# Optimization experiments

Hardware: AMD Instinct MI355X
Metric: run time of the kernel (lower is better)

Reference implementation:

```python
import jax, jax.numpy as jnp
import numpy as np


def setup_inputs() -> dict:
    key = jax.random.key(0)
    B, N = 128, 512
    SSMap = jax.random.normal(key, (B, N, N), dtype=jnp.float32)
    return {"SSMap": SSMap}


def reference(SSMap):
    # SSMap: [B, N, N]. For each superdiagonal offset d = 1..N-2 (length L = N-d,
    # the final length-1 diagonal is excluded), compute unbiased std of
    # (diag * L / 5) = std(diag) * L / 5, then mean over diagonals per batch item.
    B, N, _ = SSMap.shape
    K = N - 2  # number of diagonals used (offsets 1..N-2)
    P = N - 1  # max diagonal length
    k = jnp.arange(K)[:, None]            # diagonal index -> offset d = k+1
    p = jnp.arange(P)[None, :]            # position along diagonal
    rows = jnp.broadcast_to(p, (K, P))    # row index i = p
    cols = p + k + 1                      # col index j = p + d
    mask = cols < N                       # valid positions: p < N - d
    cols = jnp.minimum(cols, N - 1)
    diags = SSMap[:, rows, cols]          # [B, K, P] padded diagonals
    maskf = mask.astype(SSMap.dtype)      # [K, P]
    lens = jnp.sum(maskf, axis=1)         # [K], L = N - 1 - k (>= 2)
    mean = jnp.sum(diags * maskf, axis=2) / lens            # [B, K]
    dev = (diags - mean[:, :, None]) * maskf                # masked deviations
    var = jnp.sum(dev * dev, axis=2) / (lens - 1.0)         # unbiased (ddof=1)
    scaled = jnp.sqrt(var) * lens / 5.0                     # std(diag * L / 5)
    loss = jnp.mean(scaled, axis=1)                         # [B]
    return (loss, jax.lax.stop_gradient(loss))
```

## Files before the change

kernel.cpp:

```cpp
#include <hip/hip_runtime.h>
#include <math.h>

constexpr int B_ = 128;
constexpr int N_ = 512;
constexpr int K_ = 510;

__global__ __launch_bounds__(512) void diag_partial_kernel(
    const float* __restrict__ in, float* __restrict__ ws, int split) {
  const int b = blockIdx.x / split;
  const int s = blockIdx.x % split;
  const int k = threadIdx.x;
  const float* base = in + (size_t)b * N_ * N_;
  float S = 0.0f, Q = 0.0f;
  if (k < K_) {
    const int limit = N_ - 1 - k;
    const float* ptr = base + (size_t)s * (N_ + 1) + 1 + k;
    for (int p = s; p < limit; p += split) {
      float x = *ptr;
      S += x;
      Q = fmaf(x, x, Q);
      ptr += (size_t)split * (N_ + 1);
    }
  }
  float* w = ws + (size_t)blockIdx.x * (2 * N_);
  w[k] = S;
  w[k + N_] = Q;
}

__global__ __launch_bounds__(512) void finalize_kernel(
    const float* __restrict__ ws, float* __restrict__ out, int split) {
  __shared__ float red[8];
  const int b = blockIdx.x;
  const int t = threadIdx.x;
  float Ssum = 0.0f, Qsum = 0.0f;
  for (int s = 0; s < split; ++s) {
    const float* w = ws + (size_t)(b * split + s) * (2 * N_);
    Ssum += w[t];
    Qsum += w[t + N_];
  }
  float scaled = 0.0f;
  if (t < K_) {
    float len = (float)(N_ - 1 - t);
    float mean = Ssum / len;
    float var = (Qsum - Ssum * mean) / (len - 1.0f);
    var = fmaxf(var, 0.0f);
    scaled = sqrtf(var) * len * 0.2f;
  }
  for (int off = 32; off > 0; off >>= 1)
    scaled += __shfl_down(scaled, off, 64);
  const int wid = t >> 6;
  if ((t & 63) == 0) red[wid] = scaled;
  __syncthreads();
  if (t == 0) {
    float tot = 0.0f;
    for (int i = 0; i < 8; ++i) tot += red[i];
    float loss = tot / (float)K_;
    out[b] = loss;
    out[B_ + b] = loss;
  }
}

extern "C" void kernel_launch(void* const* d_in, const int* in_sizes, int n_in,
                              void* d_out, int out_size, void* d_ws, size_t ws_size,
                              hipStream_t stream) {
  const float* in = (const float*)d_in[0];
  float* out = (float*)d_out;
  float* ws = (float*)d_ws;
  int split = 8;
  while (split > 1 &&
         (size_t)B_ * split * 2 * N_ * sizeof(float) > ws_size)
    split >>= 1;
  diag_partial_kernel<<<B_ * split, 512, 0, stream>>>(in, ws, split);
  finalize_kernel<<<B_, 512, 0, stream>>>(ws, out, split);
}
```

Baseline: 196.8 us.

## Pair long and short diagonals per thread, unroll loads, double the split

Each thread now handles two diagonals, one long (offset t+1) and one short (length t), so every thread in a block does about the same amount of work. Blocks shrink to 256 threads. The main loop is unrolled by four with separate accumulators so several independent loads are in flight at once. The split factor rises from 8 to 16 to launch more blocks, at the cost of a larger workspace and more partial sums for the finalize kernel to add up.

```diff
diff --git a/kernel.cpp b/kernel.cpp
--- a/kernel.cpp
+++ b/kernel.cpp
@@ -5,26 +5,56 @@
 constexpr int N_ = 512;
 constexpr int K_ = 510;
 
-__global__ __launch_bounds__(512) void diag_partial_kernel(
+__global__ __launch_bounds__(256) void diag_partial_kernel(
     const float* __restrict__ in, float* __restrict__ ws, int split) {
   const int b = blockIdx.x / split;
   const int s = blockIdx.x % split;
-  const int k = threadIdx.x;
+  const int t = threadIdx.x;
   const float* base = in + (size_t)b * N_ * N_;
-  float S = 0.0f, Q = 0.0f;
-  if (k < K_) {
-    const int limit = N_ - 1 - k;
-    const float* ptr = base + (size_t)s * (N_ + 1) + 1 + k;
-    for (int p = s; p < limit; p += split) {
-      float x = *ptr;
-      S += x;
-      Q = fmaf(x, x, Q);
-      ptr += (size_t)split * (N_ + 1);
+  const int la = (N_ - 1) - t;
+  const int lb = t;
+  const size_t step = (size_t)split * (N_ + 1);
+  const float* pa = base + (size_t)s * (N_ + 1) + 1 + t;
+  const float* pb = base + (size_t)s * (N_ + 1) + (N_ - t);
+  float Sa0 = 0.f, Qa0 = 0.f, Sa1 = 0.f, Qa1 = 0.f;
+  float Sb0 = 0.f, Qb0 = 0.f, Sb1 = 0.f, Qb1 = 0.f;
+  int p = s;
+  for (; p + 3 * split < la; p += 4 * split) {
+    float a0 = pa[0];
+    float a1 = pa[step];
+    float a2 = pa[2 * step];
+    float a3 = pa[3 * step];
+    float b0 = 0.f, b1 = 0.f, b2 = 0.f, b3 = 0.f;
+    if (p < lb)             b0 = pb[0];
+    if (p + split < lb)     b1 = pb[step];
+    if (p + 2 * split < lb) b2 = pb[2 * step];
+    if (p + 3 * split < lb) b3 = pb[3 * step];
+    Sa0 += a0; Qa0 = fmaf(a0, a0, Qa0);
+    Sa1 += a1; Qa1 = fmaf(a1, a1, Qa1);
+    Sa0 += a2; Qa0 = fmaf(a2, a2, Qa0);
+    Sa1 += a3; Qa1 = fmaf(a3, a3, Qa1);
+    Sb0 += b0; Qb0 = fmaf(b0, b0, Qb0);
+    Sb1 += b1; Qb1 = fmaf(b1, b1, Qb1);
+    Sb0 += b2; Qb0 = fmaf(b2, b2, Qb0);
+    Sb1 += b3; Qb1 = fmaf(b3, b3, Qb1);
+    pa += 4 * step;
+    pb += 4 * step;
+  }
+  for (; p < la; p += split) {
+    float a0 = pa[0];
+    Sa0 += a0; Qa0 = fmaf(a0, a0, Qa0);
+    if (p < lb) {
+      float b0 = pb[0];
+      Sb0 += b0; Qb0 = fmaf(b0, b0, Qb0);
     }
+    pa += step;
+    pb += step;
   }
   float* w = ws + (size_t)blockIdx.x * (2 * N_);
-  w[k] = S;
-  w[k + N_] = Q;
+  w[t] = Sa0 + Sa1;
+  w[t + N_] = Qa0 + Qa1;
+  w[(N_ - 1) - t] = Sb0 + Sb1;
+  w[(N_ - 1) - t + N_] = Qb0 + Qb1;
 }
 
 __global__ __launch_bounds__(512) void finalize_kernel(
@@ -66,10 +96,10 @@
   const float* in = (const float*)d_in[0];
   float* out = (float*)d_out;
   float* ws = (float*)d_ws;
-  int split = 8;
+  int split = 16;
   while (split > 1 &&
          (size_t)B_ * split * 2 * N_ * sizeof(float) > ws_size)
     split >>= 1;
-  diag_partial_kernel<<<B_ * split, 512, 0, stream>>>(in, ws, split);
+  diag_partial_kernel<<<B_ * split, 256, 0, stream>>>(in, ws, split);
   finalize_kernel<<<B_, 512, 0, stream>>>(ws, out, split);
 }
```

Result: faster. 181.5 us (-7.8%).
